# Optimization experiments

Hardware: AMD Instinct MI355X
Metric: run time of the kernel (lower is better)

Reference implementation:

```python
import jax, jax.numpy as jnp
import numpy as np

KS = 3          # kernel_size
M = 6           # num_bases
TEM = 6         # tem_size = (KS//2)*num_bases
BN_EPS = 1e-3   # keras BatchNormalization default epsilon


def _conv(x, w):
    # x: NCHW, w: OIHW, stride 1, SAME padding (module uses padding='same')
    return jax.lax.conv_general_dilated(x, w, (1, 1), 'SAME',
                                        dimension_numbers=('NCHW', 'OIHW', 'NCHW'))


def _bn(x, gamma, beta, mean, var):
    # inference-mode batchnorm over channel dim (NCHW)
    s = gamma * jax.lax.rsqrt(var + BN_EPS)
    return x * s[None, :, None, None] + (beta - mean * s)[None, :, None, None]


def _unfold(x):
    # im2col: N,C,H,W -> N,C,KS*KS,H,W with SAME padding, stride 1
    N, C, H, W = x.shape
    xp = jnp.pad(x, ((0, 0), (0, 0), (1, 1), (1, 1)))
    taps = [xp[:, :, i:i + H, j:j + W] for i in range(KS) for j in range(KS)]
    return jnp.stack(taps, axis=2)


def setup_inputs() -> dict:
    key = jax.random.key(0)
    ks = jax.random.split(key, 16)
    N, C, O, H, W = 16, 128, 128, 64, 64
    inter, bsz = 64, M * TEM  # 64, 36
    x = jax.random.normal(ks[0], (N, C, H, W), jnp.float32)
    w1 = jax.random.normal(ks[1], (inter, C, 3, 3), jnp.float32) * (1.0 / np.sqrt(C * 9))
    gamma1 = jnp.ones((inter,), jnp.float32)
    beta1 = jnp.zeros((inter,), jnp.float32)
    mean1 = jax.random.normal(ks[2], (inter,), jnp.float32) * 0.1
    var1 = jax.random.uniform(ks[3], (inter,), jnp.float32, 0.5, 1.5)
    w2 = jax.random.normal(ks[4], (bsz, inter, 3, 3), jnp.float32) * (1.0 / np.sqrt(inter * 9))
    gamma2 = jnp.ones((bsz,), jnp.float32)
    beta2 = jnp.zeros((bsz,), jnp.float32)
    mean2 = jax.random.normal(ks[5], (bsz,), jnp.float32) * 0.1
    var2 = jax.random.uniform(ks[6], (bsz,), jnp.float32, 0.5, 1.5)
    # Fixed Fourier-Bessel-style basis [TEM, KS*KS], normalized as in calculate_FB_bases
    rng = np.random.RandomState(0)
    psi = rng.normal(size=(KS * KS, TEM)).astype(np.float32)
    c = np.sqrt((psi ** 2).sum(0).mean())
    fb_bases = jnp.asarray((psi / c).T)  # [TEM, 9]
    coef = jax.random.normal(ks[7], (O, C * M), jnp.float32) * np.sqrt(2.0 / (C * M))
    bias = jnp.zeros((O,), jnp.float32)
    return {'x': x, 'w1': w1, 'gamma1': gamma1, 'beta1': beta1, 'mean1': mean1,
            'var1': var1, 'w2': w2, 'gamma2': gamma2, 'beta2': beta2,
            'mean2': mean2, 'var2': var2, 'fb_bases': fb_bases, 'coef': coef,
            'bias': bias}


def reference(x, w1, gamma1, beta1, mean1, var1, w2, gamma2, beta2, mean2, var2,
              fb_bases, coef, bias):
    N, C, H, W = x.shape
    # bases_net: conv3x3 -> BN -> tanh -> conv3x3 -> BN -> tanh
    h = jnp.tanh(_bn(_conv(x, w1), gamma1, beta1, mean1, var1))
    b = jnp.tanh(_bn(_conv(h, w2), gamma2, beta2, mean2, var2))   # N,36,H,W
    bcoef = b.reshape(N, M, TEM, H, W)
    # combine predicted coefficients with fixed FB bases -> per-pixel filters
    bases = jnp.einsum('bmkhw,kl->bmlhw', bcoef, fb_bases)        # N,M,9,H,W
    xu = _unfold(x)                                               # N,C,9,H,W
    # per-pixel gather-multiply-reduce over the 9 taps
    bo = jnp.einsum('bmlhw,bclhw->bcmhw', bases, xu)              # N,C,M,H,W
    bo = bo.reshape(N, C * M, H, W)
    # 1x1 conv with coef + bias
    out = jnp.einsum('bkhw,ok->bohw', bo, coef) + bias[None, :, None, None]
    return out
```

## Files before the change

kernel.cpp:

```cpp
#include <hip/hip_runtime.h>
#include <hip/hip_bf16.h>

using bf16 = __hip_bfloat16;
typedef __attribute__((ext_vector_type(8))) short bf16x8;
typedef __attribute__((ext_vector_type(4))) float f32x4;
typedef __attribute__((ext_vector_type(2))) float f32x2;

#define BN_EPS 1e-3f

#define OFF_FLAG  0u
#define OFF_W1M   16u
#define OFF_B1F   36880u
#define OFF_W2M   36944u
#define OFF_B2F   50768u
#define OFF_FBF   50804u
#define OFF_CFM   50860u
#define OFF_BIASF 100012u
#define OFF_BB    100144u

__device__ __forceinline__ float b2f(bf16 v) { return __bfloat162float(v); }
__device__ __forceinline__ unsigned short f2b(float f) {
    union { bf16 h; unsigned short u; } cv;
    cv.h = __float2bfloat16(f);
    return cv.u;
}
__device__ __forceinline__ unsigned packbf(float a, float b) {
    return (unsigned)f2b(a) | ((unsigned)f2b(b) << 16);
}
__device__ __forceinline__ float ldin(const void* p, long long i, int f) {
    return f ? b2f(((const bf16*)p)[i]) : ((const float*)p)[i];
}
__device__ __forceinline__ float lo_f(unsigned u) { return __uint_as_float(u << 16); }
__device__ __forceinline__ float hi_f(unsigned u) { return __uint_as_float(u & 0xFFFF0000u); }
__device__ __forceinline__ void ld8f(const void* p, long long i, int f, float* o) {
    if (f) {
        uint4 v = *(const uint4*)((const unsigned short*)p + i);
        o[0] = lo_f(v.x); o[1] = hi_f(v.x); o[2] = lo_f(v.y); o[3] = hi_f(v.y);
        o[4] = lo_f(v.z); o[5] = hi_f(v.z); o[6] = lo_f(v.w); o[7] = hi_f(v.w);
    } else {
        const float* q = (const float*)p + i;
        float4 a = *(const float4*)q, b = *(const float4*)(q + 4);
        o[0] = a.x; o[1] = a.y; o[2] = a.z; o[3] = a.w;
        o[4] = b.x; o[5] = b.y; o[6] = b.z; o[7] = b.w;
    }
}
__device__ __forceinline__ bf16x8 lds_frag(const unsigned short* p) {
    uint2 lo = *(const uint2*)p;
    uint2 hi = *(const uint2*)(p + 4);
    union { unsigned u[4]; bf16x8 v; } r;
    r.u[0] = lo.x; r.u[1] = lo.y; r.u[2] = hi.x; r.u[3] = hi.y;
    return r.v;
}

__global__ void detect_kernel(const void* __restrict__ g1, float* __restrict__ ws) {
    if (threadIdx.x == 0) {
        unsigned w = ((const unsigned*)g1)[0];
        ws[OFF_FLAG] = (w == 0x3F800000u) ? 0.f : 1.f;
    }
}

__global__ __launch_bounds__(256) void prep_kernel(
    const void* __restrict__ w1, const void* __restrict__ g1, const void* __restrict__ be1,
    const void* __restrict__ mu1, const void* __restrict__ va1,
    const void* __restrict__ w2, const void* __restrict__ g2, const void* __restrict__ be2,
    const void* __restrict__ mu2, const void* __restrict__ va2,
    const void* __restrict__ fb, const void* __restrict__ coef, const void* __restrict__ bias,
    float* __restrict__ ws)
{
    const int f = (ws[OFF_FLAG] != 0.f);
    int j = blockIdx.x * 256 + threadIdx.x;
    if (j < 73728) {
        int tap = j >> 13, r = j & 8191;
        int ntile = r >> 11, r2 = r & 2047;
        int ks = r2 >> 9, r3 = r2 & 511;
        int lane = r3 >> 3, jj = r3 & 7;
        int oc = ntile * 16 + (lane & 15);
        int ic = ks * 32 + (lane >> 4) * 8 + jj;
        float s = ldin(g1, oc, f) * rsqrtf(ldin(va1, oc, f) + BN_EPS);
        ((unsigned short*)(ws + OFF_W1M))[j] = f2b(ldin(w1, (oc * 128 + ic) * 9 + tap, f) * s);
        return;
    }
    j -= 73728;
    if (j < 64) {
        float s = ldin(g1, j, f) * rsqrtf(ldin(va1, j, f) + BN_EPS);
        ws[OFF_B1F + j] = ldin(be1, j, f) - ldin(mu1, j, f) * s;
        return;
    }
    j -= 64;
    if (j < 27648) {
        int tap = j / 3072, r = j - tap * 3072;
        int ntile = r >> 10, r2 = r & 1023;
        int ks = r2 >> 9, r3 = r2 & 511;
        int lane = r3 >> 3, jj = r3 & 7;
        int oc = ntile * 16 + (lane & 15);
        int ic = ks * 32 + (lane >> 4) * 8 + jj;
        float v = 0.f;
        if (oc < 36) {
            float s = ldin(g2, oc, f) * rsqrtf(ldin(va2, oc, f) + BN_EPS);
            v = ldin(w2, (oc * 64 + ic) * 9 + tap, f) * s;
        }
        ((unsigned short*)(ws + OFF_W2M))[j] = f2b(v);
        return;
    }
    j -= 27648;
    if (j < 36) {
        float s = ldin(g2, j, f) * rsqrtf(ldin(va2, j, f) + BN_EPS);
        ws[OFF_B2F + j] = ldin(be2, j, f) - ldin(mu2, j, f) * s;
        return;
    }
    j -= 36;
    if (j < 54) { ws[OFF_FBF + j] = ldin(fb, j, f); return; }
    j -= 54;
    if (j < 98304) {
        int chunk = j / 12288, r = j - chunk * 12288;
        int ks = r >> 12, r2 = r & 4095;
        int ntile = r2 >> 9, r3 = r2 & 511;
        int lane = r3 >> 3, jj = r3 & 7;
        int o = ntile * 16 + (lane & 15);
        int k = chunk * 96 + ks * 32 + (lane >> 4) * 8 + jj;
        ((unsigned short*)(ws + OFF_CFM))[j] = f2b(ldin(coef, o * 768 + k, f));
        return;
    }
    j -= 98304;
    if (j < 128) { ws[OFF_BIASF + j] = ldin(bias, j, f); return; }
}

__global__ __launch_bounds__(512, 8) void conv1_mfma(
    const void* __restrict__ x, const float* __restrict__ ws,
    unsigned short* __restrict__ hbuf)
{
    __shared__ unsigned short sA[3][66][132];
    unsigned* sAu = (unsigned*)sA;
    const unsigned short* w1m = (const unsigned short*)(ws + OFF_W1M);
    const int f = (ws[OFF_FLAG] != 0.f);
    const int t = threadIdx.x;
    const int n = blockIdx.x >> 6, h = blockIdx.x & 63;

    for (int e = t; e < 396; e += 512) {
        int dy = e / 132, q = e - dy * 132;
        int wrow = (q >= 66) ? 65 : 0;
        int cu = (q >= 66) ? q - 66 : q;
        sAu[(dy * 66 + wrow) * 66 + cu] = 0u;
    }
    {
        const long long xb = (long long)n * 128 * 4096;
        for (int u = t; u < 1536; u += 512) {
            int dy = u >> 9, rem = u & 511, icp = rem >> 3, w8 = rem & 7;
            int hh = h + dy - 1;
            float va[8], vb[8];
            if (hh >= 0 && hh < 64) {
                long long base = xb + (long long)(icp * 2) * 4096 + hh * 64 + w8 * 8;
                ld8f(x, base, f, va);
                ld8f(x, base + 4096, f, vb);
            } else {
#pragma unroll
                for (int i = 0; i < 8; ++i) { va[i] = 0.f; vb[i] = 0.f; }
            }
            const int wb_ = w8 * 8 + 1;
#pragma unroll
            for (int i = 0; i < 8; ++i)
                sAu[(dy * 66 + wb_ + i) * 66 + icp] = packbf(va[i], vb[i]);
        }
    }
    __syncthreads();

    const int wv = t >> 6, lane = t & 63;
    const int fr = lane & 15, quad = lane >> 4;
    const int mh = (wv & 3) * 16;
    const int nh = (wv >> 2) * 32;
    const int ntb = nh >> 4;

    f32x4 acc[2];
#pragma unroll
    for (int j = 0; j < 2; ++j) acc[j] = (f32x4){0.f, 0.f, 0.f, 0.f};

#pragma unroll
    for (int tap = 0; tap < 9; ++tap) {
        const int dy = tap / 3, dx = tap - dy * 3;
#pragma unroll
        for (int ks = 0; ks < 4; ++ks) {
            const int kof = ks * 32 + quad * 8;
            bf16x8 a = lds_frag(&sA[dy][mh + fr + dx][kof]);
            bf16x8 b0 = *(const bf16x8*)(w1m + (((tap * 4 + ntb) * 4 + ks) * 64 + lane) * 8);
            bf16x8 b1 = *(const bf16x8*)(w1m + (((tap * 4 + ntb + 1) * 4 + ks) * 64 + lane) * 8);
            acc[0] = __builtin_amdgcn_mfma_f32_16x16x32_bf16(a, b0, acc[0], 0, 0, 0);
            acc[1] = __builtin_amdgcn_mfma_f32_16x16x32_bf16(a, b1, acc[1], 0, 0, 0);
        }
    }

#pragma unroll
    for (int nt = 0; nt < 2; ++nt) {
        int oc = nh + nt * 16 + fr;
        int m0 = mh + quad * 4;
        float bv = ws[OFF_B1F + oc];
        f32x4 v = acc[nt];
        union { unsigned short us[4]; uint2 u; } pk;
#pragma unroll
        for (int i = 0; i < 4; ++i) pk.us[i] = f2b(tanhf(v[i] + bv));
        *(uint2*)(hbuf + (size_t)(n * 64 + oc) * 4096 + h * 64 + m0) = pk.u;
    }
}

__global__ __launch_bounds__(512, 8) void conv2_mfma(
    const float* __restrict__ ws, const unsigned short* __restrict__ hbuf,
    float* __restrict__ bbout)
{
    __shared__ unsigned short sA[3][66][68];
    unsigned* sAu = (unsigned*)sA;
    const unsigned short* w2m = (const unsigned short*)(ws + OFF_W2M);
    const int t = threadIdx.x;
    const int n = blockIdx.x >> 6, h = blockIdx.x & 63;

    for (int e = t; e < 204; e += 512) {
        int dy = e / 68, q = e - dy * 68;
        int wrow = (q >= 34) ? 65 : 0;
        int cu = (q >= 34) ? q - 34 : q;
        sAu[(dy * 66 + wrow) * 34 + cu] = 0u;
    }
    {
        const unsigned short* hn = hbuf + (size_t)n * 64 * 4096;
        for (int u = t; u < 768; u += 512) {
            int dy = u >> 8, rem = u & 255, icp = rem >> 3, w8 = rem & 7;
            int hh = h + dy - 1;
            uint4 a = make_uint4(0u, 0u, 0u, 0u), b = a;
            if (hh >= 0 && hh < 64) {
                const unsigned short* p = hn + (size_t)(icp * 2) * 4096 + hh * 64 + w8 * 8;
                a = *(const uint4*)p;
                b = *(const uint4*)(p + 4096);
            }
            const int wb_ = w8 * 8 + 1;
            unsigned au[4] = {a.x, a.y, a.z, a.w}, bu[4] = {b.x, b.y, b.z, b.w};
#pragma unroll
            for (int jj = 0; jj < 4; ++jj) {
                unsigned lo = (au[jj] & 0xFFFFu) | (bu[jj] << 16);
                unsigned hi = (au[jj] >> 16) | (bu[jj] & 0xFFFF0000u);
                sAu[(dy * 66 + wb_ + 2 * jj) * 34 + icp] = lo;
                sAu[(dy * 66 + wb_ + 2 * jj + 1) * 34 + icp] = hi;
            }
        }
    }
    __syncthreads();

    const int wv = t >> 6, lane = t & 63;
    const int fr = lane & 15, quad = lane >> 4;
    const int m0 = (wv & 3) * 16;
    const int ngrp = wv >> 2;

    f32x4 acc[2];
#pragma unroll
    for (int i = 0; i < 2; ++i) acc[i] = (f32x4){0.f, 0.f, 0.f, 0.f};

#pragma unroll
    for (int tap = 0; tap < 9; ++tap) {
        const int dy = tap / 3, dx = tap - dy * 3;
#pragma unroll
        for (int ks = 0; ks < 2; ++ks) {
            const int kof = ks * 32 + quad * 8;
            bf16x8 a = lds_frag(&sA[dy][m0 + fr + dx][kof]);
            if (ngrp == 0) {
                bf16x8 b0 = *(const bf16x8*)(w2m + (((tap * 3 + 0) * 2 + ks) * 64 + lane) * 8);
                bf16x8 b1 = *(const bf16x8*)(w2m + (((tap * 3 + 1) * 2 + ks) * 64 + lane) * 8);
                acc[0] = __builtin_amdgcn_mfma_f32_16x16x32_bf16(a, b0, acc[0], 0, 0, 0);
                acc[1] = __builtin_amdgcn_mfma_f32_16x16x32_bf16(a, b1, acc[1], 0, 0, 0);
            } else {
                bf16x8 b2 = *(const bf16x8*)(w2m + (((tap * 3 + 2) * 2 + ks) * 64 + lane) * 8);
                acc[0] = __builtin_amdgcn_mfma_f32_16x16x32_bf16(a, b2, acc[0], 0, 0, 0);
            }
        }
    }

    const int pbase = (n << 12) + h * 64 + m0 + quad * 4;
    if (ngrp == 0) {
#pragma unroll
        for (int nt = 0; nt < 2; ++nt) {
            int oc = nt * 16 + fr;
            float bv = ws[OFF_B2F + oc];
            f32x4 v = acc[nt];
#pragma unroll
            for (int reg = 0; reg < 4; ++reg)
                bbout[(size_t)(pbase + reg) * 36 + oc] = tanhf(v[reg] + bv);
        }
    } else {
        int oc = 32 + fr;
        if (oc < 36) {
            float bv = ws[OFF_B2F + oc];
            f32x4 v = acc[0];
#pragma unroll
            for (int reg = 0; reg < 4; ++reg)
                bbout[(size_t)(pbase + reg) * 36 + oc] = tanhf(v[reg] + bv);
        }
    }
}

__global__ __launch_bounds__(512, 8) void fuse_kernel(
    const void* __restrict__ x, const float* __restrict__ ws, void* __restrict__ outv)
{
    __shared__ float sbT[64][60];
    __shared__ __align__(16) unsigned short slbo[64][104];
    __shared__ __align__(16) unsigned short sX[3][66][20];
    unsigned* sXu = (unsigned*)sX;

    const float* bbp = ws + OFF_BB;
    const float* fbf = ws + OFF_FBF;
    const unsigned short* cfm = (const unsigned short*)(ws + OFF_CFM);
    const int f = (ws[OFF_FLAG] != 0.f);

    const int t = threadIdx.x;
    const int p0 = blockIdx.x * 64;
    const int n = p0 >> 12;
    const int h = (p0 >> 6) & 63;

    const long long xbase = (long long)n * 128 * 4096;
    const int sw = t & 63, sg = t >> 6;

    float rv0[3], rv1[3];
#pragma unroll
    for (int dy = 0; dy < 3; ++dy) {
        int hh = h + dy - 1;
        float v0 = 0.f, v1 = 0.f;
        if (hh >= 0 && hh < 64) {
            long long base = xbase + (long long)(sg * 2) * 4096 + hh * 64 + sw;
            v0 = ldin(x, base, f);
            v1 = ldin(x, base + 4096, f);
        }
        rv0[dy] = v0; rv1[dy] = v1;
    }

    for (int task = t; task < 64 * 54; task += 512) {
        int p = task & 63, j = task >> 6;
        int m = j / 9, l = j - m * 9;
        const float* br = bbp + (size_t)(p0 + p) * 36 + m * 6;
        float s = 0.f;
#pragma unroll
        for (int k = 0; k < 6; ++k) s += br[k] * fbf[k * 9 + l];
        sbT[p][l * 6 + m] = s;
    }
    if (t < 48) {
        int dy = t >> 4, q = t & 15;
        int wrow = (q >= 8) ? 65 : 0;
        sXu[(dy * 66 + wrow) * 10 + (q & 7)] = 0u;
    }

    const int pp = t >> 3, cl = t & 7;
    const int wv = t >> 6, lane = t & 63;
    const int fr = lane & 15, quad = lane >> 4;
    const int m0w = (wv & 3) * 16;
    const int nh = (wv >> 2) * 64;
    const int ntb = nh >> 4;

    f32x4 acc[4];
#pragma unroll
    for (int nt = 0; nt < 4; ++nt) acc[nt] = (f32x4){0.f, 0.f, 0.f, 0.f};

    __syncthreads();

#pragma unroll
    for (int chunk = 0; chunk < 8; ++chunk) {
#pragma unroll
        for (int dy = 0; dy < 3; ++dy)
            sXu[(dy * 66 + sw + 1) * 10 + sg] = packbf(rv0[dy], rv1[dy]);
        __syncthreads();
        if (chunk < 7) {
            const int c0n = (chunk + 1) * 16;
#pragma unroll
            for (int dy = 0; dy < 3; ++dy) {
                int hh = h + dy - 1;
                float v0 = 0.f, v1 = 0.f;
                if (hh >= 0 && hh < 64) {
                    long long base = xbase + (long long)(c0n + sg * 2) * 4096 + hh * 64 + sw;
                    v0 = ldin(x, base, f);
                    v1 = ldin(x, base + 4096, f);
                }
                rv0[dy] = v0; rv1[dy] = v1;
            }
        }
        {
            f32x2 xv[9];
#pragma unroll
            for (int dy = 0; dy < 3; ++dy)
#pragma unroll
                for (int dx = 0; dx < 3; ++dx) {
                    unsigned d = sXu[(dy * 66 + pp + dx) * 10 + cl];
                    xv[dy * 3 + dx] = (f32x2){lo_f(d), hi_f(d)};
                }
            f32x2 sm2[6];
#pragma unroll
            for (int m = 0; m < 6; ++m) sm2[m] = (f32x2){0.f, 0.f};
            const float* sp = &sbT[pp][0];
#pragma unroll
            for (int jv = 0; jv < 13; ++jv) {
                f32x4 s4 = *(const f32x4*)(sp + jv * 4);
#pragma unroll
                for (int e = 0; e < 4; ++e) {
                    const int j = jv * 4 + e;
                    const int l = j / 6, m = j - l * 6;
                    sm2[m] += xv[l] * s4[e];
                }
            }
            {
                f32x2 s2 = *(const f32x2*)(sp + 52);
                sm2[4] += xv[8] * s2[0];
                sm2[5] += xv[8] * s2[1];
            }
            unsigned* du = (unsigned*)slbo + pp * 52 + cl * 6;
            uint2 w0 = make_uint2(packbf(sm2[0][0], sm2[1][0]), packbf(sm2[2][0], sm2[3][0]));
            uint2 w1 = make_uint2(packbf(sm2[4][0], sm2[5][0]), packbf(sm2[0][1], sm2[1][1]));
            uint2 w2 = make_uint2(packbf(sm2[2][1], sm2[3][1]), packbf(sm2[4][1], sm2[5][1]));
            *(uint2*)&du[0] = w0;
            *(uint2*)&du[2] = w1;
            *(uint2*)&du[4] = w2;
        }
        __syncthreads();
#pragma unroll
        for (int ks = 0; ks < 3; ++ks) {
            const int kof = ks * 32 + quad * 8;
            bf16x8 a = *(const bf16x8*)&slbo[m0w + fr][kof];
            const unsigned short* cb = cfm + ((chunk * 3 + ks) * 8 + ntb) * 512 + lane * 8;
            bf16x8 b0 = *(const bf16x8*)(cb);
            bf16x8 b1 = *(const bf16x8*)(cb + 512);
            bf16x8 b2 = *(const bf16x8*)(cb + 1024);
            bf16x8 b3 = *(const bf16x8*)(cb + 1536);
            acc[0] = __builtin_amdgcn_mfma_f32_16x16x32_bf16(a, b0, acc[0], 0, 0, 0);
            acc[1] = __builtin_amdgcn_mfma_f32_16x16x32_bf16(a, b1, acc[1], 0, 0, 0);
            acc[2] = __builtin_amdgcn_mfma_f32_16x16x32_bf16(a, b2, acc[2], 0, 0, 0);
            acc[3] = __builtin_amdgcn_mfma_f32_16x16x32_bf16(a, b3, acc[3], 0, 0, 0);
        }
    }

    const int mrow = m0w + quad * 4;
#pragma unroll
    for (int nt = 0; nt < 4; ++nt) {
        int o = nh + nt * 16 + fr;
        float bv = ws[OFF_BIASF + o];
        f32x4 v = acc[nt];
        size_t ofs = (size_t)(n * 128 + o) * 4096 + h * 64 + mrow;
        if (f) {
            union { unsigned short us[4]; uint2 u; } pk;
#pragma unroll
            for (int i = 0; i < 4; ++i) pk.us[i] = f2b(v[i] + bv);
            *(uint2*)((unsigned short*)outv + ofs) = pk.u;
        } else {
            float4 w4 = make_float4(v[0] + bv, v[1] + bv, v[2] + bv, v[3] + bv);
            *(float4*)((float*)outv + ofs) = w4;
        }
    }
}

extern "C" void kernel_launch(void* const* d_in, const int* in_sizes, int n_in,
                              void* d_out, int out_size, void* d_ws, size_t ws_size,
                              hipStream_t stream)
{
    float* ws = (float*)d_ws;
    unsigned short* hbuf = (unsigned short*)d_out;

    hipLaunchKernelGGL(detect_kernel, dim3(1), dim3(64), 0, stream, d_in[2], ws);
    hipLaunchKernelGGL(prep_kernel, dim3(782), dim3(256), 0, stream,
                       d_in[1], d_in[2], d_in[3], d_in[4], d_in[5],
                       d_in[6], d_in[7], d_in[8], d_in[9], d_in[10],
                       d_in[11], d_in[12], d_in[13], ws);
    hipLaunchKernelGGL(conv1_mfma, dim3(1024), dim3(512), 0, stream, d_in[0], ws, hbuf);
    hipLaunchKernelGGL(conv2_mfma, dim3(1024), dim3(512), 0, stream, ws, hbuf, ws + OFF_BB);
    hipLaunchKernelGGL(fuse_kernel, dim3(1024), dim3(512), 0, stream, d_in[0], ws, d_out);
}
```

Measured before the change: 201.7 us.

## Fuse conv2 into the fuse kernel and keep basis coefficients in LDS

```diff
diff --git a/kernel.cpp b/kernel.cpp
--- a/kernel.cpp
+++ b/kernel.cpp
@@ -16,7 +16,7 @@
 #define OFF_FBF   50804u
 #define OFF_CFM   50860u
 #define OFF_BIASF 100012u
-#define OFF_BB    100144u
+#define OFF_HBUF  100144u
 
 __device__ __forceinline__ float b2f(bf16 v) { return __bfloat162float(v); }
 __device__ __forceinline__ unsigned short f2b(float f) {
@@ -125,7 +125,7 @@
     if (j < 128) { ws[OFF_BIASF + j] = ldin(bias, j, f); return; }
 }
 
-__global__ __launch_bounds__(512, 8) void conv1_mfma(
+__global__ __launch_bounds__(512, 6) void conv1_mfma(
     const void* __restrict__ x, const float* __restrict__ ws,
     unsigned short* __restrict__ hbuf)
 {
@@ -201,21 +201,52 @@
     }
 }
 
-__global__ __launch_bounds__(512, 8) void conv2_mfma(
-    const float* __restrict__ ws, const unsigned short* __restrict__ hbuf,
-    float* __restrict__ bbout)
+__global__ __launch_bounds__(512, 6) void fuse_kernel(
+    const void* __restrict__ x, const float* __restrict__ ws,
+    const unsigned short* __restrict__ hbuf, void* __restrict__ outv)
 {
-    __shared__ unsigned short sA[3][66][68];
-    unsigned* sAu = (unsigned*)sA;
+    __shared__ float sbT[64][60];
+    __shared__ __align__(16) unsigned char Rb[37440];
+    unsigned* sHu = (unsigned*)Rb;
+    unsigned short* sHs = (unsigned short*)Rb;
+    float* sb36 = (float*)(Rb + 26928);
+    unsigned* sXu = (unsigned*)Rb;
+    unsigned short* slbo = (unsigned short*)(Rb + 7936);
+
+    const float* fbf = ws + OFF_FBF;
+    const unsigned short* cfm = (const unsigned short*)(ws + OFF_CFM);
     const unsigned short* w2m = (const unsigned short*)(ws + OFF_W2M);
+    const int f = (ws[OFF_FLAG] != 0.f);
+
     const int t = threadIdx.x;
-    const int n = blockIdx.x >> 6, h = blockIdx.x & 63;
+    const int p0 = blockIdx.x * 64;
+    const int n = p0 >> 12;
+    const int h = (p0 >> 6) & 63;
+
+    const int wv = t >> 6, lane = t & 63;
+    const int fr = lane & 15, quad = lane >> 4;
+
+    const long long xbase = (long long)n * 128 * 4096;
+    const int sw = t & 63, sg = t >> 6;
+
+    float rv0[3], rv1[3];
+#pragma unroll
+    for (int dy = 0; dy < 3; ++dy) {
+        int hh = h + dy - 1;
+        float v0 = 0.f, v1 = 0.f;
+        if (hh >= 0 && hh < 64) {
+            long long base = xbase + (long long)(sg * 2) * 4096 + hh * 64 + sw;
+            v0 = ldin(x, base, f);
+            v1 = ldin(x, base + 4096, f);
+        }
+        rv0[dy] = v0; rv1[dy] = v1;
+    }
 
     for (int e = t; e < 204; e += 512) {
         int dy = e / 68, q = e - dy * 68;
         int wrow = (q >= 34) ? 65 : 0;
         int cu = (q >= 34) ? q - 34 : q;
-        sAu[(dy * 66 + wrow) * 34 + cu] = 0u;
+        sHu[(dy * 66 + wrow) * 34 + cu] = 0u;
     }
     {
         const unsigned short* hn = hbuf + (size_t)n * 64 * 4096;
@@ -234,102 +265,63 @@
             for (int jj = 0; jj < 4; ++jj) {
                 unsigned lo = (au[jj] & 0xFFFFu) | (bu[jj] << 16);
                 unsigned hi = (au[jj] >> 16) | (bu[jj] & 0xFFFF0000u);
-                sAu[(dy * 66 + wb_ + 2 * jj) * 34 + icp] = lo;
-                sAu[(dy * 66 + wb_ + 2 * jj + 1) * 34 + icp] = hi;
+                sHu[(dy * 66 + wb_ + 2 * jj) * 34 + icp] = lo;
+                sHu[(dy * 66 + wb_ + 2 * jj + 1) * 34 + icp] = hi;
             }
         }
     }
     __syncthreads();
 
-    const int wv = t >> 6, lane = t & 63;
-    const int fr = lane & 15, quad = lane >> 4;
-    const int m0 = (wv & 3) * 16;
-    const int ngrp = wv >> 2;
-
-    f32x4 acc[2];
-#pragma unroll
-    for (int i = 0; i < 2; ++i) acc[i] = (f32x4){0.f, 0.f, 0.f, 0.f};
-
-#pragma unroll
-    for (int tap = 0; tap < 9; ++tap) {
-        const int dy = tap / 3, dx = tap - dy * 3;
-#pragma unroll
-        for (int ks = 0; ks < 2; ++ks) {
-            const int kof = ks * 32 + quad * 8;
-            bf16x8 a = lds_frag(&sA[dy][m0 + fr + dx][kof]);
-            if (ngrp == 0) {
-                bf16x8 b0 = *(const bf16x8*)(w2m + (((tap * 3 + 0) * 2 + ks) * 64 + lane) * 8);
-                bf16x8 b1 = *(const bf16x8*)(w2m + (((tap * 3 + 1) * 2 + ks) * 64 + lane) * 8);
-                acc[0] = __builtin_amdgcn_mfma_f32_16x16x32_bf16(a, b0, acc[0], 0, 0, 0);
-                acc[1] = __builtin_amdgcn_mfma_f32_16x16x32_bf16(a, b1, acc[1], 0, 0, 0);
-            } else {
-                bf16x8 b2 = *(const bf16x8*)(w2m + (((tap * 3 + 2) * 2 + ks) * 64 + lane) * 8);
-                acc[0] = __builtin_amdgcn_mfma_f32_16x16x32_bf16(a, b2, acc[0], 0, 0, 0);
-            }
-        }
-    }
-
-    const int pbase = (n << 12) + h * 64 + m0 + quad * 4;
-    if (ngrp == 0) {
-#pragma unroll
-        for (int nt = 0; nt < 2; ++nt) {
-            int oc = nt * 16 + fr;
+    {
+        const int m0c = (wv & 3) * 16;
+        const int ngrp = wv >> 2;
+        f32x4 c2[2];
+        c2[0] = (f32x4){0.f, 0.f, 0.f, 0.f};
+        c2[1] = (f32x4){0.f, 0.f, 0.f, 0.f};
+#pragma unroll
+        for (int tap = 0; tap < 9; ++tap) {
+            const int dy = tap / 3, dx = tap - dy * 3;
+#pragma unroll
+            for (int ks = 0; ks < 2; ++ks) {
+                const int kof = ks * 32 + quad * 8;
+                bf16x8 a = lds_frag(&sHs[((dy * 66 + m0c + fr + dx)) * 68 + kof]);
+                if (ngrp == 0) {
+                    bf16x8 b0 = *(const bf16x8*)(w2m + (((tap * 3 + 0) * 2 + ks) * 64 + lane) * 8);
+                    bf16x8 b1 = *(const bf16x8*)(w2m + (((tap * 3 + 1) * 2 + ks) * 64 + lane) * 8);
+                    c2[0] = __builtin_amdgcn_mfma_f32_16x16x32_bf16(a, b0, c2[0], 0, 0, 0);
+                    c2[1] = __builtin_amdgcn_mfma_f32_16x16x32_bf16(a, b1, c2[1], 0, 0, 0);
+                } else {
+                    bf16x8 b2 = *(const bf16x8*)(w2m + (((tap * 3 + 2) * 2 + ks) * 64 + lane) * 8);
+                    c2[0] = __builtin_amdgcn_mfma_f32_16x16x32_bf16(a, b2, c2[0], 0, 0, 0);
+                }
+            }
+        }
+        const int pb = m0c + quad * 4;
+        if (ngrp == 0) {
+#pragma unroll
+            for (int nt = 0; nt < 2; ++nt) {
+                int oc = nt * 16 + fr;
+                float bv = ws[OFF_B2F + oc];
+                f32x4 v = c2[nt];
+#pragma unroll
+                for (int reg = 0; reg < 4; ++reg)
+                    sb36[(pb + reg) * 41 + oc] = tanhf(v[reg] + bv);
+            }
+        } else if (fr < 4) {
+            int oc = 32 + fr;
             float bv = ws[OFF_B2F + oc];
-            f32x4 v = acc[nt];
+            f32x4 v = c2[0];
 #pragma unroll
             for (int reg = 0; reg < 4; ++reg)
-                bbout[(size_t)(pbase + reg) * 36 + oc] = tanhf(v[reg] + bv);
-        }
-    } else {
-        int oc = 32 + fr;
-        if (oc < 36) {
-            float bv = ws[OFF_B2F + oc];
-            f32x4 v = acc[0];
-#pragma unroll
-            for (int reg = 0; reg < 4; ++reg)
-                bbout[(size_t)(pbase + reg) * 36 + oc] = tanhf(v[reg] + bv);
-        }
-    }
-}
-
-__global__ __launch_bounds__(512, 8) void fuse_kernel(
-    const void* __restrict__ x, const float* __restrict__ ws, void* __restrict__ outv)
-{
-    __shared__ float sbT[64][60];
-    __shared__ __align__(16) unsigned short slbo[64][104];
-    __shared__ __align__(16) unsigned short sX[3][66][20];
-    unsigned* sXu = (unsigned*)sX;
-
-    const float* bbp = ws + OFF_BB;
-    const float* fbf = ws + OFF_FBF;
-    const unsigned short* cfm = (const unsigned short*)(ws + OFF_CFM);
-    const int f = (ws[OFF_FLAG] != 0.f);
-
-    const int t = threadIdx.x;
-    const int p0 = blockIdx.x * 64;
-    const int n = p0 >> 12;
-    const int h = (p0 >> 6) & 63;
-
-    const long long xbase = (long long)n * 128 * 4096;
-    const int sw = t & 63, sg = t >> 6;
-
-    float rv0[3], rv1[3];
-#pragma unroll
-    for (int dy = 0; dy < 3; ++dy) {
-        int hh = h + dy - 1;
-        float v0 = 0.f, v1 = 0.f;
-        if (hh >= 0 && hh < 64) {
-            long long base = xbase + (long long)(sg * 2) * 4096 + hh * 64 + sw;
-            v0 = ldin(x, base, f);
-            v1 = ldin(x, base + 4096, f);
-        }
-        rv0[dy] = v0; rv1[dy] = v1;
-    }
+                sb36[(pb + reg) * 41 + oc] = tanhf(v[reg] + bv);
+        }
+    }
+    __syncthreads();
 
     for (int task = t; task < 64 * 54; task += 512) {
         int p = task & 63, j = task >> 6;
         int m = j / 9, l = j - m * 9;
-        const float* br = bbp + (size_t)(p0 + p) * 36 + m * 6;
+        const float* br = sb36 + p * 41 + m * 6;
         float s = 0.f;
 #pragma unroll
         for (int k = 0; k < 6; ++k) s += br[k] * fbf[k * 9 + l];
@@ -342,8 +334,6 @@
     }
 
     const int pp = t >> 3, cl = t & 7;
-    const int wv = t >> 6, lane = t & 63;
-    const int fr = lane & 15, quad = lane >> 4;
     const int m0w = (wv & 3) * 16;
     const int nh = (wv >> 2) * 64;
     const int ntb = nh >> 4;
@@ -414,7 +404,7 @@
 #pragma unroll
         for (int ks = 0; ks < 3; ++ks) {
             const int kof = ks * 32 + quad * 8;
-            bf16x8 a = *(const bf16x8*)&slbo[m0w + fr][kof];
+            bf16x8 a = *(const bf16x8*)(slbo + (m0w + fr) * 104 + kof);
             const unsigned short* cb = cfm + ((chunk * 3 + ks) * 8 + ntb) * 512 + lane * 8;
             bf16x8 b0 = *(const bf16x8*)(cb);
             bf16x8 b1 = *(const bf16x8*)(cb + 512);
@@ -451,7 +441,7 @@
                               hipStream_t stream)
 {
     float* ws = (float*)d_ws;
-    unsigned short* hbuf = (unsigned short*)d_out;
+    unsigned short* hbuf = (unsigned short*)(ws + OFF_HBUF);
 
     hipLaunchKernelGGL(detect_kernel, dim3(1), dim3(64), 0, stream, d_in[2], ws);
     hipLaunchKernelGGL(prep_kernel, dim3(782), dim3(256), 0, stream,
@@ -459,6 +449,5 @@
                        d_in[6], d_in[7], d_in[8], d_in[9], d_in[10],
                        d_in[11], d_in[12], d_in[13], ws);
     hipLaunchKernelGGL(conv1_mfma, dim3(1024), dim3(512), 0, stream, d_in[0], ws, hbuf);
-    hipLaunchKernelGGL(conv2_mfma, dim3(1024), dim3(512), 0, stream, ws, hbuf, ws + OFF_BB);
-    hipLaunchKernelGGL(fuse_kernel, dim3(1024), dim3(512), 0, stream, d_in[0], ws, d_out);
-}
+    hipLaunchKernelGGL(fuse_kernel, dim3(1024), dim3(512), 0, stream, d_in[0], ws, hbuf, d_out);
+}
```

Result: slower. 214.2 us (+6.2%).
